# Kernel optimization log

Hardware: AMD Instinct MI355X
Metric: run time of the kernel (lower is better)

The kernel has to match this reference:

```python
import jax, jax.numpy as jnp
import numpy as np

NUM_GENES = 9229
NUM_FEATURES = 3
BATCH = 4096


def setup_inputs() -> dict:
    key = jax.random.key(0)
    k1, k2, k3 = jax.random.split(key, 3)
    x = jax.random.normal(k1, (BATCH, NUM_GENES * NUM_FEATURES), dtype=jnp.float32)
    weights = jax.random.normal(k2, (NUM_GENES * NUM_FEATURES,), dtype=jnp.float32)
    bias = 0.1 * jax.random.normal(k3, (NUM_GENES,), dtype=jnp.float32)
    return {"x": x, "weights": weights, "bias": bias}


def reference(x, weights, bias):
    # Block-diagonal scatter + mm is equivalent to a per-gene weighted sum
    # over the feature dimension:
    # x: [B, G*F] -> [B, G, F]; weights: [G*F] -> [G, F]
    B = x.shape[0]
    xg = x.reshape(B, NUM_GENES, NUM_FEATURES)
    wg = weights.reshape(NUM_GENES, NUM_FEATURES)
    out = jnp.einsum("bgf,gf->bg", xg, wg) + bias  # [B, G]
    return out
```

## Files before the change

kernel.cpp:

```cpp
#include <hip/hip_runtime.h>


#define G     9229
#define GF    27687
#define NB    4096
#define NWIN  36
#define SLOTS 221
#define NW    (37 * SLOTS)

typedef float f32x4 __attribute__((ext_vector_type(4)));

__global__ __launch_bounds__(256) void diag_layer_kernel(
    const float* __restrict__ x,
    const float* __restrict__ w,
    const float* __restrict__ bias,
    float* __restrict__ out) {

    const int t = (int)(threadIdx.x & 63);
    const int W = (int)blockIdx.x * 4 + (int)(threadIdx.x >> 6);
    if (W >= NW) return;
    const int win = W % 37;
    const int s   = W / 37;

    if (win < NWIN) {
        const int F0 = 768 * win;
        const float4 w0 = *reinterpret_cast<const float4*>(w + F0 + 4 * t);
        const float4 w1 = *reinterpret_cast<const float4*>(w + F0 + 256 + 4 * t);
        const float4 w2 = *reinterpret_cast<const float4*>(w + F0 + 512 + 4 * t);
        const float4 bv = *reinterpret_cast<const float4*>(bias + 256 * win + 4 * t);

        const int tm   = t % 3;
        const bool last = (t == 63);
        const int srcA = (3 * t) & 63;
        const int srcC = (3 * t + 1) & 63;
        const int srcD = (3 * t + 2) & 63;

#pragma unroll 2
        for (int r = s; r < NB; r += SLOTS) {
            const float* xr = x + r * GF + F0;
            const f32x4 v0 = __builtin_nontemporal_load(
                reinterpret_cast<const f32x4*>(xr + 4 * t));
            const f32x4 v1 = __builtin_nontemporal_load(
                reinterpret_cast<const f32x4*>(xr + 256 + 4 * t));
            const f32x4 v2 = __builtin_nontemporal_load(
                reinterpret_cast<const f32x4*>(xr + 512 + 4 * t));

            const float a0 = v0.x * w0.x, a1 = v0.y * w0.y, a2 = v0.z * w0.z, a3 = v0.w * w0.w;
            const float q01_0 = a0 + a1, q23_0 = a2 + a3;
            const float q012_0 = q01_0 + a2, q123_0 = q23_0 + a1;
            const float b0 = v1.x * w1.x, b1 = v1.y * w1.y, b2 = v1.z * w1.z, b3 = v1.w * w1.w;
            const float q01_1 = b0 + b1, q23_1 = b2 + b3;
            const float q012_1 = q01_1 + b2, q123_1 = q23_1 + b1;
            const float c0 = v2.x * w2.x, c1 = v2.y * w2.y, c2 = v2.z * w2.z, c3 = v2.w * w2.w;
            const float q01_2 = c0 + c1, q23_2 = c2 + c3;
            const float q012_2 = q01_2 + c2, q123_2 = q23_2 + c1;

            const float s0 = (tm == 1) ? q01_0 : a0;
            const float s1 = (tm == 0) ? q01_1 : b0;
            const float s2 = (tm == 2) ? q01_2 : c0;
            const float r0 = __shfl(s0, (t + 1) & 63);
            const float r1 = __shfl(s1, (t + 1) & 63);
            const float r2 = __shfl(s2, (t + 1) & 63);
            const float E0 = last ? r1 : r0;
            const float E1 = last ? r2 : r1;
            const float E2 = r2;

            const float bb0 = a3 + E0, bb1 = b3 + E1, bb2 = c3 + E2;
            const float cc0 = q23_0 + E0, cc1 = q23_1 + E1, cc2 = q23_2 + E2;

            const float A  = (tm == 0) ? q012_0 : (tm == 2) ? q012_1 : q012_2;
            const float Bv = (tm == 0) ? bb0   : (tm == 2) ? bb1   : bb2;
            const float C  = (tm == 1) ? cc0   : (tm == 0) ? cc1   : cc2;
            const float D  = (tm == 2) ? q123_0 : (tm == 1) ? q123_1 : q123_2;

            f32x4 o;
            o.x = __shfl(A,  srcA) + bv.x;
            o.y = __shfl(Bv, srcA) + bv.y;
            o.z = __shfl(C,  srcC) + bv.z;
            o.w = __shfl(D,  srcD) + bv.w;

            __builtin_nontemporal_store(
                o, reinterpret_cast<f32x4*>(out + r * G + 256 * win + 4 * t));
        }
    } else {
        if (t < 13) {
            const int g = 9216 + t;
            const float wa = w[3 * g], wb = w[3 * g + 1], wc = w[3 * g + 2];
            const float bz = bias[g];
            for (int r = s; r < NB; r += SLOTS) {
                const float* xr = x + r * GF + 3 * g;
                out[r * G + g] =
                    fmaf(xr[0], wa, fmaf(xr[1], wb, fmaf(xr[2], wc, bz)));
            }
        }
    }
}

extern "C" void kernel_launch(void* const* d_in, const int* in_sizes, int n_in,
                              void* d_out, int out_size, void* d_ws, size_t ws_size,
                              hipStream_t stream) {
    const float* x    = (const float*)d_in[0];
    const float* w    = (const float*)d_in[1];
    const float* bias = (const float*)d_in[2];
    float* out        = (float*)d_out;

    diag_layer_kernel<<<2048, 256, 0, stream>>>(x, w, bias, out);
}
```

Measured before the change: 120.6 us.

## Process the output as flat 256-element units using wrap-extended weight and bias copies

Treats the whole output (B*G) as one flat array split into 256-gene units, each fed by a contiguous 768-float slice of x. A small pre-kernel builds weight and bias arrays in the workspace, extended with a wrapped copy, so units that cross a row boundary still read the right values. This removes the scalar tail path for the last 13 genes and balances work across waves. The cost is an extra launch plus per-unit weight and bias loads, which replace the register-resident weights of the old version. If the workspace is too small, the code falls back to the old kernel.

```diff
diff --git a/kernel.cpp b/kernel.cpp
--- a/kernel.cpp
+++ b/kernel.cpp
@@ -1,97 +1,164 @@
 #include <hip/hip_runtime.h>
 
 
-#define G     9229
-#define GF    27687
+#define G       9229
+#define GFW     27687
+#define NUNIT   147664
+#define NWAVES  8192
+#define WEXT_N  (GFW + 768)
+#define BEXT_OFF 28456
+#define BEXT_N  (G + 256)
+#define WS_FLOATS (BEXT_OFF + BEXT_N)
+
+typedef float f32x4 __attribute__((ext_vector_type(4)));
+
+__global__ __launch_bounds__(256) void build_ext_kernel(
+    const float* __restrict__ w, const float* __restrict__ bias,
+    float* __restrict__ ws) {
+    const int i = (int)blockIdx.x * 256 + (int)threadIdx.x;
+    if (i < WEXT_N) {
+        ws[i] = w[i >= GFW ? i - GFW : i];
+    } else {
+        const int k = i - WEXT_N;
+        if (k < BEXT_N) ws[BEXT_OFF + k] = bias[k >= G ? k - G : k];
+    }
+}
+
+__global__ __launch_bounds__(256, 8) void diag_flat_kernel(
+    const float* __restrict__ x,
+    const float* __restrict__ ws,
+    float* __restrict__ out) {
+
+    const float* wext = ws;
+    const float* bext = ws + BEXT_OFF;
+
+    const int t  = (int)(threadIdx.x & 63);
+    const int wv = (int)blockIdx.x * 4 + (int)(threadIdx.x >> 6);
+
+    const int tm    = t % 3;
+    const bool last = (t == 63);
+    const int srcA = (3 * t) & 63;
+    const int srcC = (3 * t + 1) & 63;
+    const int srcD = (3 * t + 2) & 63;
+
+    for (unsigned u = (unsigned)wv; u < NUNIT; u += NWAVES) {
+        const unsigned O0  = 256u * u;
+        const unsigned g0  = O0 % (unsigned)G;
+        const unsigned wf0 = 3u * g0;
+        const float* xr = x + 768u * u;
+
+        const f32x4 v0 = __builtin_nontemporal_load(
+            reinterpret_cast<const f32x4*>(xr + 4 * t));
+        const f32x4 v1 = __builtin_nontemporal_load(
+            reinterpret_cast<const f32x4*>(xr + 256 + 4 * t));
+        const f32x4 v2 = __builtin_nontemporal_load(
+            reinterpret_cast<const f32x4*>(xr + 512 + 4 * t));
+
+        const float4 w0 = *reinterpret_cast<const float4*>(wext + wf0 + 4 * t);
+        const float4 w1 = *reinterpret_cast<const float4*>(wext + wf0 + 256 + 4 * t);
+        const float4 w2 = *reinterpret_cast<const float4*>(wext + wf0 + 512 + 4 * t);
+        const float4 bv = *reinterpret_cast<const float4*>(bext + g0 + 4 * t);
+
+        const float a0 = v0.x * w0.x, a1 = v0.y * w0.y, a2 = v0.z * w0.z, a3 = v0.w * w0.w;
+        const float q01_0 = a0 + a1, q23_0 = a2 + a3;
+        const float q012_0 = q01_0 + a2, q123_0 = q23_0 + a1;
+        const float b0 = v1.x * w1.x, b1 = v1.y * w1.y, b2 = v1.z * w1.z, b3 = v1.w * w1.w;
+        const float q01_1 = b0 + b1, q23_1 = b2 + b3;
+        const float q012_1 = q01_1 + b2, q123_1 = q23_1 + b1;
+        const float c0 = v2.x * w2.x, c1 = v2.y * w2.y, c2 = v2.z * w2.z, c3 = v2.w * w2.w;
+        const float q01_2 = c0 + c1, q23_2 = c2 + c3;
+        const float q012_2 = q01_2 + c2, q123_2 = q23_2 + c1;
+
+        const float s0 = (tm == 1) ? q01_0 : a0;
+        const float s1 = (tm == 0) ? q01_1 : b0;
+        const float s2 = (tm == 2) ? q01_2 : c0;
+        const float r0 = __shfl(s0, (t + 1) & 63);
+        const float r1 = __shfl(s1, (t + 1) & 63);
+        const float r2 = __shfl(s2, (t + 1) & 63);
+        const float E0 = last ? r1 : r0;
+        const float E1 = last ? r2 : r1;
+        const float E2 = r2;
+
+        const float bb0 = a3 + E0, bb1 = b3 + E1, bb2 = c3 + E2;
+        const float cc0 = q23_0 + E0, cc1 = q23_1 + E1, cc2 = q23_2 + E2;
+
+        const float A  = (tm == 0) ? q012_0 : (tm == 2) ? q012_1 : q012_2;
+        const float Bv = (tm == 0) ? bb0   : (tm == 2) ? bb1   : bb2;
+        const float C  = (tm == 1) ? cc0   : (tm == 0) ? cc1   : cc2;
+        const float D  = (tm == 2) ? q123_0 : (tm == 1) ? q123_1 : q123_2;
+
+        f32x4 o;
+        o.x = __shfl(A,  srcA) + bv.x;
+        o.y = __shfl(Bv, srcA) + bv.y;
+        o.z = __shfl(C,  srcC) + bv.z;
+        o.w = __shfl(D,  srcD) + bv.w;
+
+        __builtin_nontemporal_store(
+            o, reinterpret_cast<f32x4*>(out + O0 + 4 * t));
+    }
+}
+
 #define NB    4096
 #define NWIN  36
 #define SLOTS 221
-#define NW    (37 * SLOTS)
+#define NWF   (37 * SLOTS)
 
-typedef float f32x4 __attribute__((ext_vector_type(4)));
-
-__global__ __launch_bounds__(256) void diag_layer_kernel(
-    const float* __restrict__ x,
-    const float* __restrict__ w,
-    const float* __restrict__ bias,
-    float* __restrict__ out) {
-
+__global__ __launch_bounds__(256) void diag_layer_kernel_fb(
+    const float* __restrict__ x, const float* __restrict__ w,
+    const float* __restrict__ bias, float* __restrict__ out) {
     const int t = (int)(threadIdx.x & 63);
     const int W = (int)blockIdx.x * 4 + (int)(threadIdx.x >> 6);
-    if (W >= NW) return;
+    if (W >= NWF) return;
     const int win = W % 37;
     const int s   = W / 37;
-
     if (win < NWIN) {
         const int F0 = 768 * win;
         const float4 w0 = *reinterpret_cast<const float4*>(w + F0 + 4 * t);
         const float4 w1 = *reinterpret_cast<const float4*>(w + F0 + 256 + 4 * t);
         const float4 w2 = *reinterpret_cast<const float4*>(w + F0 + 512 + 4 * t);
         const float4 bv = *reinterpret_cast<const float4*>(bias + 256 * win + 4 * t);
-
-        const int tm   = t % 3;
+        const int tm = t % 3;
         const bool last = (t == 63);
-        const int srcA = (3 * t) & 63;
-        const int srcC = (3 * t + 1) & 63;
-        const int srcD = (3 * t + 2) & 63;
-
+        const int srcA = (3 * t) & 63, srcC = (3 * t + 1) & 63, srcD = (3 * t + 2) & 63;
 #pragma unroll 2
         for (int r = s; r < NB; r += SLOTS) {
-            const float* xr = x + r * GF + F0;
-            const f32x4 v0 = __builtin_nontemporal_load(
-                reinterpret_cast<const f32x4*>(xr + 4 * t));
-            const f32x4 v1 = __builtin_nontemporal_load(
-                reinterpret_cast<const f32x4*>(xr + 256 + 4 * t));
-            const f32x4 v2 = __builtin_nontemporal_load(
-                reinterpret_cast<const f32x4*>(xr + 512 + 4 * t));
-
+            const float* xr = x + r * GFW + F0;
+            const f32x4 v0 = __builtin_nontemporal_load(reinterpret_cast<const f32x4*>(xr + 4 * t));
+            const f32x4 v1 = __builtin_nontemporal_load(reinterpret_cast<const f32x4*>(xr + 256 + 4 * t));
+            const f32x4 v2 = __builtin_nontemporal_load(reinterpret_cast<const f32x4*>(xr + 512 + 4 * t));
             const float a0 = v0.x * w0.x, a1 = v0.y * w0.y, a2 = v0.z * w0.z, a3 = v0.w * w0.w;
-            const float q01_0 = a0 + a1, q23_0 = a2 + a3;
-            const float q012_0 = q01_0 + a2, q123_0 = q23_0 + a1;
+            const float q01_0 = a0 + a1, q23_0 = a2 + a3, q012_0 = a0 + a1 + a2, q123_0 = q23_0 + a1;
             const float b0 = v1.x * w1.x, b1 = v1.y * w1.y, b2 = v1.z * w1.z, b3 = v1.w * w1.w;
-            const float q01_1 = b0 + b1, q23_1 = b2 + b3;
-            const float q012_1 = q01_1 + b2, q123_1 = q23_1 + b1;
+            const float q01_1 = b0 + b1, q23_1 = b2 + b3, q012_1 = q01_1 + b2, q123_1 = q23_1 + b1;
             const float c0 = v2.x * w2.x, c1 = v2.y * w2.y, c2 = v2.z * w2.z, c3 = v2.w * w2.w;
-            const float q01_2 = c0 + c1, q23_2 = c2 + c3;
-            const float q012_2 = q01_2 + c2, q123_2 = q23_2 + c1;
-
+            const float q01_2 = c0 + c1, q23_2 = c2 + c3, q012_2 = q01_2 + c2, q123_2 = q23_2 + c1;
             const float s0 = (tm == 1) ? q01_0 : a0;
             const float s1 = (tm == 0) ? q01_1 : b0;
             const float s2 = (tm == 2) ? q01_2 : c0;
             const float r0 = __shfl(s0, (t + 1) & 63);
             const float r1 = __shfl(s1, (t + 1) & 63);
             const float r2 = __shfl(s2, (t + 1) & 63);
-            const float E0 = last ? r1 : r0;
-            const float E1 = last ? r2 : r1;
-            const float E2 = r2;
-
+            const float E0 = last ? r1 : r0, E1 = last ? r2 : r1, E2 = r2;
             const float bb0 = a3 + E0, bb1 = b3 + E1, bb2 = c3 + E2;
             const float cc0 = q23_0 + E0, cc1 = q23_1 + E1, cc2 = q23_2 + E2;
-
             const float A  = (tm == 0) ? q012_0 : (tm == 2) ? q012_1 : q012_2;
-            const float Bv = (tm == 0) ? bb0   : (tm == 2) ? bb1   : bb2;
-            const float C  = (tm == 1) ? cc0   : (tm == 0) ? cc1   : cc2;
+            const float Bv = (tm == 0) ? bb0 : (tm == 2) ? bb1 : bb2;
+            const float C  = (tm == 1) ? cc0 : (tm == 0) ? cc1 : cc2;
             const float D  = (tm == 2) ? q123_0 : (tm == 1) ? q123_1 : q123_2;
-
             f32x4 o;
-            o.x = __shfl(A,  srcA) + bv.x;
+            o.x = __shfl(A, srcA) + bv.x;
             o.y = __shfl(Bv, srcA) + bv.y;
-            o.z = __shfl(C,  srcC) + bv.z;
-            o.w = __shfl(D,  srcD) + bv.w;
-
-            __builtin_nontemporal_store(
-                o, reinterpret_cast<f32x4*>(out + r * G + 256 * win + 4 * t));
+            o.z = __shfl(C, srcC) + bv.z;
+            o.w = __shfl(D, srcD) + bv.w;
+            __builtin_nontemporal_store(o, reinterpret_cast<f32x4*>(out + r * G + 256 * win + 4 * t));
         }
-    } else {
-        if (t < 13) {
-            const int g = 9216 + t;
-            const float wa = w[3 * g], wb = w[3 * g + 1], wc = w[3 * g + 2];
-            const float bz = bias[g];
-            for (int r = s; r < NB; r += SLOTS) {
-                const float* xr = x + r * GF + 3 * g;
-                out[r * G + g] =
-                    fmaf(xr[0], wa, fmaf(xr[1], wb, fmaf(xr[2], wc, bz)));
-            }
+    } else if (t < 13) {
+        const int g = 9216 + t;
+        const float wa = w[3 * g], wb = w[3 * g + 1], wc = w[3 * g + 2];
+        const float bz = bias[g];
+        for (int r = s; r < NB; r += SLOTS) {
+            const float* xr = x + r * GFW + 3 * g;
+            out[r * G + g] = fmaf(xr[0], wa, fmaf(xr[1], wb, fmaf(xr[2], wc, bz)));
         }
     }
 }
@@ -104,5 +171,11 @@
     const float* bias = (const float*)d_in[2];
     float* out        = (float*)d_out;
 
-    diag_layer_kernel<<<2048, 256, 0, stream>>>(x, w, bias, out);
+    if (ws_size >= WS_FLOATS * sizeof(float)) {
+        float* ws = (float*)d_ws;
+        build_ext_kernel<<<(WEXT_N + BEXT_N + 255) / 256, 256, 0, stream>>>(w, bias, ws);
+        diag_flat_kernel<<<2048, 256, 0, stream>>>(x, ws, out);
+    } else {
+        diag_layer_kernel_fb<<<2048, 256, 0, stream>>>(x, w, bias, out);
+    }
 }
```

Result: no change. 119.0 us (-1.3%).

## Flatten output into uniform 256-element units with per-unit wrapped weight loads

Applied to the files above, without the earlier changes.

Replaces the row-by-window decomposition with a flat split of the output into equal 256-element units, each reading a contiguous 768-float slab of x. This removes the separate scalar tail path for the last 13 genes and spreads work evenly across all waves, two units per iteration. In exchange, every unit reloads its weights and bias at a gene offset that is generally not 16-byte aligned. Units that cross a row boundary take a slower per-element path that wraps the gene index.

```diff
diff --git a/kernel.cpp b/kernel.cpp
--- a/kernel.cpp
+++ b/kernel.cpp
@@ -1,98 +1,130 @@
 #include <hip/hip_runtime.h>
 
 
-#define G     9229
-#define GF    27687
-#define NB    4096
-#define NWIN  36
-#define SLOTS 221
-#define NW    (37 * SLOTS)
+#define G      9229u
+#define GFW    27687u
+#define NUNIT  147664u
+#define NWAVES 8192u
 
 typedef float f32x4 __attribute__((ext_vector_type(4)));
 
-__global__ __launch_bounds__(256) void diag_layer_kernel(
+__device__ __forceinline__ void load_wb(
+    const float* __restrict__ w, const float* __restrict__ bias,
+    unsigned g0, int t,
+    float4& w0, float4& w1, float4& w2, float4& bv) {
+    const unsigned wf0 = 3u * g0;
+    if (g0 <= 8973u) {
+        w0 = *reinterpret_cast<const float4*>(w + wf0 + 4 * t);
+        w1 = *reinterpret_cast<const float4*>(w + wf0 + 256 + 4 * t);
+        w2 = *reinterpret_cast<const float4*>(w + wf0 + 512 + 4 * t);
+        bv = *reinterpret_cast<const float4*>(bias + g0 + 4 * t);
+    } else {
+        float wt[12], bt[4];
+#pragma unroll
+        for (int c = 0; c < 4; ++c) {
+            unsigned i0 = wf0 + 4u * t + c;        if (i0 >= GFW) i0 -= GFW;
+            unsigned i1 = wf0 + 256u + 4u * t + c; if (i1 >= GFW) i1 -= GFW;
+            unsigned i2 = wf0 + 512u + 4u * t + c; if (i2 >= GFW) i2 -= GFW;
+            wt[c] = w[i0]; wt[4 + c] = w[i1]; wt[8 + c] = w[i2];
+            unsigned ib = g0 + 4u * t + c;         if (ib >= G) ib -= G;
+            bt[c] = bias[ib];
+        }
+        w0 = make_float4(wt[0], wt[1], wt[2], wt[3]);
+        w1 = make_float4(wt[4], wt[5], wt[6], wt[7]);
+        w2 = make_float4(wt[8], wt[9], wt[10], wt[11]);
+        bv = make_float4(bt[0], bt[1], bt[2], bt[3]);
+    }
+}
+
+__device__ __forceinline__ void compute_store(
+    f32x4 v0, f32x4 v1, f32x4 v2,
+    float4 w0, float4 w1, float4 w2, float4 bv,
+    int t, int tm, bool last, int srcA, int srcC, int srcD,
+    float* __restrict__ dst) {
+    const float a0 = v0.x * w0.x, a1 = v0.y * w0.y, a2 = v0.z * w0.z, a3 = v0.w * w0.w;
+    const float q01_0 = a0 + a1, q23_0 = a2 + a3;
+    const float q012_0 = q01_0 + a2, q123_0 = q23_0 + a1;
+    const float b0 = v1.x * w1.x, b1 = v1.y * w1.y, b2 = v1.z * w1.z, b3 = v1.w * w1.w;
+    const float q01_1 = b0 + b1, q23_1 = b2 + b3;
+    const float q012_1 = q01_1 + b2, q123_1 = q23_1 + b1;
+    const float c0 = v2.x * w2.x, c1 = v2.y * w2.y, c2 = v2.z * w2.z, c3 = v2.w * w2.w;
+    const float q01_2 = c0 + c1, q23_2 = c2 + c3;
+    const float q012_2 = q01_2 + c2, q123_2 = q23_2 + c1;
+
+    const float s0 = (tm == 1) ? q01_0 : a0;
+    const float s1 = (tm == 0) ? q01_1 : b0;
+    const float s2 = (tm == 2) ? q01_2 : c0;
+    const float r0 = __shfl(s0, (t + 1) & 63);
+    const float r1 = __shfl(s1, (t + 1) & 63);
+    const float r2 = __shfl(s2, (t + 1) & 63);
+    const float E0 = last ? r1 : r0;
+    const float E1 = last ? r2 : r1;
+    const float E2 = r2;
+
+    const float bb0 = a3 + E0, bb1 = b3 + E1, bb2 = c3 + E2;
+    const float cc0 = q23_0 + E0, cc1 = q23_1 + E1, cc2 = q23_2 + E2;
+
+    const float A  = (tm == 0) ? q012_0 : (tm == 2) ? q012_1 : q012_2;
+    const float Bv = (tm == 0) ? bb0   : (tm == 2) ? bb1   : bb2;
+    const float C  = (tm == 1) ? cc0   : (tm == 0) ? cc1   : cc2;
+    const float D  = (tm == 2) ? q123_0 : (tm == 1) ? q123_1 : q123_2;
+
+    f32x4 o;
+    o.x = __shfl(A,  srcA) + bv.x;
+    o.y = __shfl(Bv, srcA) + bv.y;
+    o.z = __shfl(C,  srcC) + bv.z;
+    o.w = __shfl(D,  srcD) + bv.w;
+    __builtin_nontemporal_store(o, reinterpret_cast<f32x4*>(dst));
+}
+
+__global__ __launch_bounds__(256) void diag_flat2_kernel(
     const float* __restrict__ x,
     const float* __restrict__ w,
     const float* __restrict__ bias,
     float* __restrict__ out) {
 
-    const int t = (int)(threadIdx.x & 63);
-    const int W = (int)blockIdx.x * 4 + (int)(threadIdx.x >> 6);
-    if (W >= NW) return;
-    const int win = W % 37;
-    const int s   = W / 37;
+    const int t  = (int)(threadIdx.x & 63);
+    const int wv = (int)blockIdx.x * 4 + (int)(threadIdx.x >> 6);
 
-    if (win < NWIN) {
-        const int F0 = 768 * win;
-        const float4 w0 = *reinterpret_cast<const float4*>(w + F0 + 4 * t);
-        const float4 w1 = *reinterpret_cast<const float4*>(w + F0 + 256 + 4 * t);
-        const float4 w2 = *reinterpret_cast<const float4*>(w + F0 + 512 + 4 * t);
-        const float4 bv = *reinterpret_cast<const float4*>(bias + 256 * win + 4 * t);
+    const int tm    = t % 3;
+    const bool last = (t == 63);
+    const int srcA = (3 * t) & 63;
+    const int srcC = (3 * t + 1) & 63;
+    const int srcD = (3 * t + 2) & 63;
 
-        const int tm   = t % 3;
-        const bool last = (t == 63);
-        const int srcA = (3 * t) & 63;
-        const int srcC = (3 * t + 1) & 63;
-        const int srcD = (3 * t + 2) & 63;
+    for (unsigned k = 0; k < 18; k += 2) {
+        const unsigned uA = (unsigned)wv + k * NWAVES;
+        const unsigned uB = uA + NWAVES;
+        const float* xrA = x + 768u * uA;
+        const float* xrB = x + 768u * uB;
 
-#pragma unroll 2
-        for (int r = s; r < NB; r += SLOTS) {
-            const float* xr = x + r * GF + F0;
-            const f32x4 v0 = __builtin_nontemporal_load(
-                reinterpret_cast<const f32x4*>(xr + 4 * t));
-            const f32x4 v1 = __builtin_nontemporal_load(
-                reinterpret_cast<const f32x4*>(xr + 256 + 4 * t));
-            const f32x4 v2 = __builtin_nontemporal_load(
-                reinterpret_cast<const f32x4*>(xr + 512 + 4 * t));
+        const f32x4 a0 = __builtin_nontemporal_load(reinterpret_cast<const f32x4*>(xrA + 4 * t));
+        const f32x4 a1 = __builtin_nontemporal_load(reinterpret_cast<const f32x4*>(xrA + 256 + 4 * t));
+        const f32x4 a2 = __builtin_nontemporal_load(reinterpret_cast<const f32x4*>(xrA + 512 + 4 * t));
+        const f32x4 b0 = __builtin_nontemporal_load(reinterpret_cast<const f32x4*>(xrB + 4 * t));
+        const f32x4 b1 = __builtin_nontemporal_load(reinterpret_cast<const f32x4*>(xrB + 256 + 4 * t));
+        const f32x4 b2 = __builtin_nontemporal_load(reinterpret_cast<const f32x4*>(xrB + 512 + 4 * t));
 
-            const float a0 = v0.x * w0.x, a1 = v0.y * w0.y, a2 = v0.z * w0.z, a3 = v0.w * w0.w;
-            const float q01_0 = a0 + a1, q23_0 = a2 + a3;
-            const float q012_0 = q01_0 + a2, q123_0 = q23_0 + a1;
-            const float b0 = v1.x * w1.x, b1 = v1.y * w1.y, b2 = v1.z * w1.z, b3 = v1.w * w1.w;
-            const float q01_1 = b0 + b1, q23_1 = b2 + b3;
-            const float q012_1 = q01_1 + b2, q123_1 = q23_1 + b1;
-            const float c0 = v2.x * w2.x, c1 = v2.y * w2.y, c2 = v2.z * w2.z, c3 = v2.w * w2.w;
-            const float q01_2 = c0 + c1, q23_2 = c2 + c3;
-            const float q012_2 = q01_2 + c2, q123_2 = q23_2 + c1;
+        float4 wA0, wA1, wA2, bvA, wB0, wB1, wB2, bvB;
+        load_wb(w, bias, (256u * uA) % G, t, wA0, wA1, wA2, bvA);
+        load_wb(w, bias, (256u * uB) % G, t, wB0, wB1, wB2, bvB);
 
-            const float s0 = (tm == 1) ? q01_0 : a0;
-            const float s1 = (tm == 0) ? q01_1 : b0;
-            const float s2 = (tm == 2) ? q01_2 : c0;
-            const float r0 = __shfl(s0, (t + 1) & 63);
-            const float r1 = __shfl(s1, (t + 1) & 63);
-            const float r2 = __shfl(s2, (t + 1) & 63);
-            const float E0 = last ? r1 : r0;
-            const float E1 = last ? r2 : r1;
-            const float E2 = r2;
+        compute_store(a0, a1, a2, wA0, wA1, wA2, bvA, t, tm, last, srcA, srcC, srcD,
+                      out + 256u * uA + 4 * t);
+        compute_store(b0, b1, b2, wB0, wB1, wB2, bvB, t, tm, last, srcA, srcC, srcD,
+                      out + 256u * uB + 4 * t);
+    }
 
-            const float bb0 = a3 + E0, bb1 = b3 + E1, bb2 = c3 + E2;
-            const float cc0 = q23_0 + E0, cc1 = q23_1 + E1, cc2 = q23_2 + E2;
-
-            const float A  = (tm == 0) ? q012_0 : (tm == 2) ? q012_1 : q012_2;
-            const float Bv = (tm == 0) ? bb0   : (tm == 2) ? bb1   : bb2;
-            const float C  = (tm == 1) ? cc0   : (tm == 0) ? cc1   : cc2;
-            const float D  = (tm == 2) ? q123_0 : (tm == 1) ? q123_1 : q123_2;
-
-            f32x4 o;
-            o.x = __shfl(A,  srcA) + bv.x;
-            o.y = __shfl(Bv, srcA) + bv.y;
-            o.z = __shfl(C,  srcC) + bv.z;
-            o.w = __shfl(D,  srcD) + bv.w;
-
-            __builtin_nontemporal_store(
-                o, reinterpret_cast<f32x4*>(out + r * G + 256 * win + 4 * t));
-        }
-    } else {
-        if (t < 13) {
-            const int g = 9216 + t;
-            const float wa = w[3 * g], wb = w[3 * g + 1], wc = w[3 * g + 2];
-            const float bz = bias[g];
-            for (int r = s; r < NB; r += SLOTS) {
-                const float* xr = x + r * GF + 3 * g;
-                out[r * G + g] =
-                    fmaf(xr[0], wa, fmaf(xr[1], wb, fmaf(xr[2], wc, bz)));
-            }
-        }
+    if (wv < (int)(NUNIT - 18u * NWAVES)) {
+        const unsigned u = 18u * NWAVES + (unsigned)wv;
+        const float* xr = x + 768u * u;
+        const f32x4 v0 = __builtin_nontemporal_load(reinterpret_cast<const f32x4*>(xr + 4 * t));
+        const f32x4 v1 = __builtin_nontemporal_load(reinterpret_cast<const f32x4*>(xr + 256 + 4 * t));
+        const f32x4 v2 = __builtin_nontemporal_load(reinterpret_cast<const f32x4*>(xr + 512 + 4 * t));
+        float4 w0, w1, w2, bv;
+        load_wb(w, bias, (256u * u) % G, t, w0, w1, w2, bv);
+        compute_store(v0, v1, v2, w0, w1, w2, bv, t, tm, last, srcA, srcC, srcD,
+                      out + 256u * u + 4 * t);
     }
 }
 
@@ -104,5 +136,5 @@
     const float* bias = (const float*)d_in[2];
     float* out        = (float*)d_out;
 
-    diag_layer_kernel<<<2048, 256, 0, stream>>>(x, w, bias, out);
+    diag_flat2_kernel<<<2048, 256, 0, stream>>>(x, w, bias, out);
 }
```

New measurement: 161.4 us. +33.8%, slower.

## Treat x as flat 768-float units with wrapped weight/bias extension and balanced wave split

Applied to the files above, without the earlier changes.

Views x and out as flat streams of 768/256-float units and uses a small prep kernel to build periodically extended copies of weights and bias in workspace, so every unit, including those crossing row boundaries, goes through the same vectorized path. This removes the separate scalar tail path for the last 13 genes, where 13 lanes did strided single-float loads. Work is split into contiguous, nearly equal ranges per wave, grouped by gene class so weights are reloaded only when the class changes. The cost is an extra kernel launch and extra index arithmetic in the inner loop. Alignment of the flat float4 loads relies on 768 and 256 being multiples of 4.

```diff
diff --git a/kernel.cpp b/kernel.cpp
--- a/kernel.cpp
+++ b/kernel.cpp
@@ -1,43 +1,67 @@
 #include <hip/hip_runtime.h>
 
 
-#define G     9229
-#define GF    27687
-#define NB    4096
-#define NWIN  36
-#define SLOTS 221
-#define NW    (37 * SLOTS)
+#define G        9229u
+#define GFW      27687u
+#define NUNIT    147664u
+#define NWAVES   8192u
+#define WEXT_N   (27687 + 768)
+#define BEXT_OFF 28456
+#define BEXT_N   (9229 + 256)
+#define WS_FLOATS (BEXT_OFF + BEXT_N)
 
 typedef float f32x4 __attribute__((ext_vector_type(4)));
 
-__global__ __launch_bounds__(256) void diag_layer_kernel(
+__global__ __launch_bounds__(256) void build_ext_kernel(
+    const float* __restrict__ w, const float* __restrict__ bias,
+    float* __restrict__ ws) {
+    const int i = (int)blockIdx.x * 256 + (int)threadIdx.x;
+    if (i < WEXT_N) {
+        ws[i] = w[i >= (int)GFW ? i - (int)GFW : i];
+    } else {
+        const int k = i - WEXT_N;
+        if (k < BEXT_N) ws[BEXT_OFF + k] = bias[k >= (int)G ? k - (int)G : k];
+    }
+}
+
+__global__ __launch_bounds__(256, 8) void diag_class_kernel(
     const float* __restrict__ x,
-    const float* __restrict__ w,
-    const float* __restrict__ bias,
+    const float* __restrict__ ws,
     float* __restrict__ out) {
 
-    const int t = (int)(threadIdx.x & 63);
-    const int W = (int)blockIdx.x * 4 + (int)(threadIdx.x >> 6);
-    if (W >= NW) return;
-    const int win = W % 37;
-    const int s   = W / 37;
+    const float* wext = ws;
+    const float* bext = ws + BEXT_OFF;
 
-    if (win < NWIN) {
-        const int F0 = 768 * win;
-        const float4 w0 = *reinterpret_cast<const float4*>(w + F0 + 4 * t);
-        const float4 w1 = *reinterpret_cast<const float4*>(w + F0 + 256 + 4 * t);
-        const float4 w2 = *reinterpret_cast<const float4*>(w + F0 + 512 + 4 * t);
-        const float4 bv = *reinterpret_cast<const float4*>(bias + 256 * win + 4 * t);
+    const int t  = (int)(threadIdx.x & 63);
+    const int wv = (int)blockIdx.x * 4 + (int)(threadIdx.x >> 6);
 
-        const int tm   = t % 3;
-        const bool last = (t == 63);
-        const int srcA = (3 * t) & 63;
-        const int srcC = (3 * t + 1) & 63;
-        const int srcD = (3 * t + 2) & 63;
+    const int tm    = t % 3;
+    const bool last = (t == 63);
+    const int srcA = (3 * t) & 63;
+    const int srcC = (3 * t + 1) & 63;
+    const int srcD = (3 * t + 2) & 63;
 
-#pragma unroll 2
-        for (int r = s; r < NB; r += SLOTS) {
-            const float* xr = x + r * GF + F0;
+    const unsigned cnt  = 18u + ((unsigned)wv < 208u ? 1u : 0u);
+    unsigned idx        = 18u * (unsigned)wv + ((unsigned)wv < 208u ? (unsigned)wv : 208u);
+    const unsigned end  = idx + cnt;
+
+    while (idx < end) {
+        const unsigned c    = idx >> 4;
+        const unsigned k0   = idx & 15u;
+        const unsigned rem  = end - (c << 4);
+        const unsigned kend = rem < 16u ? rem : 16u;
+        const unsigned g0   = (256u * c) % G;
+        const unsigned wf0  = 3u * g0;
+
+        const float4 w0 = *reinterpret_cast<const float4*>(wext + wf0 + 4 * t);
+        const float4 w1 = *reinterpret_cast<const float4*>(wext + wf0 + 256 + 4 * t);
+        const float4 w2 = *reinterpret_cast<const float4*>(wext + wf0 + 512 + 4 * t);
+        const float4 bv = *reinterpret_cast<const float4*>(bext + g0 + 4 * t);
+
+        for (unsigned k = k0; k < kend; ++k) {
+            const unsigned u  = c + G * k;
+            const float* xr   = x + 768u * u;
+
             const f32x4 v0 = __builtin_nontemporal_load(
                 reinterpret_cast<const f32x4*>(xr + 4 * t));
             const f32x4 v1 = __builtin_nontemporal_load(
@@ -80,19 +104,9 @@
             o.w = __shfl(D,  srcD) + bv.w;
 
             __builtin_nontemporal_store(
-                o, reinterpret_cast<f32x4*>(out + r * G + 256 * win + 4 * t));
+                o, reinterpret_cast<f32x4*>(out + 256u * u + 4 * t));
         }
-    } else {
-        if (t < 13) {
-            const int g = 9216 + t;
-            const float wa = w[3 * g], wb = w[3 * g + 1], wc = w[3 * g + 2];
-            const float bz = bias[g];
-            for (int r = s; r < NB; r += SLOTS) {
-                const float* xr = x + r * GF + 3 * g;
-                out[r * G + g] =
-                    fmaf(xr[0], wa, fmaf(xr[1], wb, fmaf(xr[2], wc, bz)));
-            }
-        }
+        idx = (c << 4) + kend;
     }
 }
 
@@ -103,6 +117,8 @@
     const float* w    = (const float*)d_in[1];
     const float* bias = (const float*)d_in[2];
     float* out        = (float*)d_out;
+    float* ws         = (float*)d_ws;
 
-    diag_layer_kernel<<<2048, 256, 0, stream>>>(x, w, bias, out);
+    build_ext_kernel<<<(WEXT_N + BEXT_N + 255) / 256, 256, 0, stream>>>(w, bias, ws);
+    diag_class_kernel<<<2048, 256, 0, stream>>>(x, ws, out);
 }
```

Result: no change. 122.0 us (+1.2%).
